# Optimization experiments

Hardware: AMD Instinct MI355X
Metric: run time of the kernel (lower is better)

The kernel has to match this reference:

```python
import jax, jax.numpy as jnp
import numpy as np

N_COMBIN, N_DEV, CONT, VOCAB, EMB = 50000, 100000, 62, 1000, 16
B, K, H, OUT, NCLS = 8192, 64, 4, 16, 1
FEAT = CONT + 2 * EMB  # 94
ALPHA = 0.2  # leaky relu slope


def setup_inputs() -> dict:
    key = jax.random.key(0)
    ks = jax.random.split(key, 32)
    rn = lambda k, shape, s=0.05: (jax.random.normal(k, shape, dtype=jnp.float32) * s)
    inp = {
        "combin_cont": jax.random.normal(ks[0], (N_COMBIN, CONT), jnp.float32),
        "combin_cat": jax.random.randint(ks[1], (N_COMBIN, 2), 0, VOCAB),
        "device_cont": jax.random.normal(ks[2], (N_DEV, CONT), jnp.float32),
        "device_cat": jax.random.randint(ks[3], (N_DEV, 2), 0, VOCAB),
        "combin_idx": jax.random.randint(ks[4], (B,), 0, N_COMBIN),
        "device_idx": jax.random.randint(ks[5], (B,), 0, N_DEV),
        "neighbor_idx": jax.random.randint(ks[6], (B, K), 0, N_DEV),
        "ce0": rn(ks[7], (VOCAB, EMB), 1.0),
        "ce1": rn(ks[8], (VOCAB, EMB), 1.0),
        "de0": rn(ks[9], (VOCAB, EMB), 1.0),
        "de1": rn(ks[10], (VOCAB, EMB), 1.0),
        "Wc": rn(ks[11], (H, FEAT, OUT)),
        "bc": rn(ks[12], (H, OUT)),
        "Wd": rn(ks[13], (H, FEAT, OUT)),
        "bd": rn(ks[14], (H, OUT)),
        "aW": rn(ks[15], (H, 2 * OUT)),
        "ab": rn(ks[16], (H,)),
        "W1": rn(ks[17], (H * OUT, OUT)),
        "b1": rn(ks[18], (OUT,)),
        "W2": rn(ks[19], (OUT + 2 * FEAT, 64)),
        "b2": rn(ks[20], (64,)),
        "W3": rn(ks[21], (64, 32)),
        "b3": rn(ks[22], (32,)),
        "W4": rn(ks[23], (32, NCLS)),
        "b4": rn(ks[24], (NCLS,)),
    }
    return inp


def reference(combin_cont, combin_cat, device_cont, device_cat,
              combin_idx, device_idx, neighbor_idx,
              ce0, ce1, de0, de1,
              Wc, bc, Wd, bd, aW, ab,
              W1, b1, W2, b2, W3, b3, W4, b4):
    # concat_embed_feats for device nodes: [N_dev, FEAT]
    dev_feats = jnp.concatenate(
        [device_cont, de0[device_cat[:, 0]], de1[device_cat[:, 1]]], axis=1)
    # combin batch features: [B, FEAT]
    cc = combin_cat[combin_idx]
    comb_batch = jnp.concatenate(
        [combin_cont[combin_idx], ce0[cc[:, 0]], ce1[cc[:, 1]]], axis=1)
    dev_batch = dev_feats[device_idx]            # [B, FEAT]
    neibr = dev_feats[neighbor_idx]              # [B, K, FEAT]

    # multi-head GAT attention (all heads vectorized)
    h_c = jnp.einsum('bf,hfo->bho', comb_batch, Wc) + bc[None]          # [B,H,OUT]
    h_n = jnp.einsum('bkf,hfo->bhko', neibr, Wd) + bd[None, :, None]    # [B,H,K,OUT]
    a1, a2 = aW[:, :OUT], aW[:, OUT:]
    e = (jnp.einsum('bho,ho->bh', h_c, a1)[:, :, None]
         + jnp.einsum('bhko,ho->bhk', h_n, a2)
         + ab[None, :, None])                                           # [B,H,K]
    e = jax.nn.leaky_relu(e, negative_slope=ALPHA)
    attn = jax.nn.softmax(e, axis=-1)
    head_out = jax.nn.elu(jnp.einsum('bhk,bhko->bho', attn, h_n))       # [B,H,OUT]
    attn_feats = head_out.reshape(head_out.shape[0], H * OUT) @ W1 + b1  # [B,OUT]

    fusion = jnp.concatenate([comb_batch, dev_batch, attn_feats], axis=1)
    x = jax.nn.relu(fusion @ W2 + b2)   # dropout is identity in eval
    x = jax.nn.relu(x @ W3 + b3)
    return jax.nn.sigmoid(x @ W4 + b4)  # [B, NCLS]
```

## Files before the change

kernel.cpp:

```cpp
#include <hip/hip_runtime.h>
#include <cmath>

#define NDEV   100000
#define NBATCH 8192
#define CONTF  62
#define EMB    16
#define FEAT   94
#define KNBR   64
#define NH     4
#define OUTD   16
#define HOUT   64
#define FUS    204
#define ALPHA  0.2f

#define NDEVG  1563
#define NCOMBG 128
#define KP     48

typedef unsigned short ushortT;
typedef unsigned int   uintT;
typedef ushortT ushort8v __attribute__((ext_vector_type(8)));
typedef short   short8  __attribute__((ext_vector_type(8)));
typedef float   float4v __attribute__((ext_vector_type(4)));


template <typename T>
__device__ __forceinline__ const T* uniform_ptr(const T* p) {
  uint64_t v = (uint64_t)(uintptr_t)p;
  uint32_t lo = __builtin_amdgcn_readfirstlane((uint32_t)v);
  uint32_t hi = __builtin_amdgcn_readfirstlane((uint32_t)(v >> 32));
  return (const T*)(uintptr_t)(((uint64_t)hi << 32) | lo);
}

__device__ __forceinline__ float bf2f(ushortT u) {
  return __uint_as_float(((unsigned int)u) << 16);
}
__device__ __forceinline__ ushortT f2bf(float f) {
  unsigned int i = __float_as_uint(f);
  unsigned int r = i + 0x7FFFu + ((i >> 16) & 1u);
  return (ushortT)(r >> 16);
}
__device__ __forceinline__ uintT pack2(float lo, float hi) {
  return ((uintT)f2bf(hi) << 16) | (uintT)f2bf(lo);
}

union FragU { uint4 u; short8 s; };

__global__ __launch_bounds__(256, 2) void k_feat(
    const float* __restrict__ device_cont, const int* __restrict__ device_cat,
    const float* __restrict__ de0, const float* __restrict__ de1,
    const float* __restrict__ Wd, const float* __restrict__ bd,
    const float* __restrict__ combin_cont, const int* __restrict__ combin_cat,
    const int* __restrict__ combin_idx,
    const float* __restrict__ ce0, const float* __restrict__ ce1,
    const float* __restrict__ Wc, const float* __restrict__ bc,
    const float* __restrict__ aW,
    ushortT* __restrict__ h_bf, float* __restrict__ e_d, float* __restrict__ e_c) {
  __shared__ uintT x_s[64 * KP];
  __shared__ uintT w_s[64 * KP];
  __shared__ int   ci_s[64];

  const int tid  = threadIdx.x;
  const int lane = tid & 63;
  const int wv = __builtin_amdgcn_readfirstlane((int)(tid >> 6));
  const int blk = blockIdx.x;
  const bool devp = blk < NDEVG;
  const int b0 = (devp ? blk : blk - NDEVG) * 64;

  if (!devp && tid < 64) ci_s[tid] = combin_idx[b0 + tid];

  {
    const float* __restrict__ Ws = devp ? Wd : Wc;
#pragma unroll 1
    for (int e = tid; e < 64 * 47; e += 256) {
      const int n = e & 63, p = e >> 6;
      const int h = n >> 4, o = n & 15;
      const float lo = Ws[(h * FEAT + 2 * p) * OUTD + o];
      const float hi = Ws[(h * FEAT + 2 * p + 1) * OUTD + o];
      w_s[n * KP + p] = pack2(lo, hi);
    }
    if (tid < 64) w_s[tid * KP + 47] = 0u;
  }
  __syncthreads();

  {
    const float* __restrict__ cont = devp ? device_cont : combin_cont;
#pragma unroll 1
    for (int e = tid; e < 64 * 31; e += 256) {
      const int r = e / 31, p = e - r * 31;
      const size_t srow = devp ? (size_t)min(b0 + r, NDEV - 1) : (size_t)ci_s[r];
      const float2 v = *reinterpret_cast<const float2*>(cont + srow * CONTF + 2 * p);
      x_s[r * KP + p] = pack2(v.x, v.y);
    }
  }
  if (tid < 128) {
    const int r = tid >> 1, tb = tid & 1;
    const int srow = devp ? min(b0 + r, NDEV - 1) : ci_s[r];
    const int cidx = (devp ? device_cat : combin_cat)[2 * srow + tb];
    const float* __restrict__ ep =
        (tb ? (devp ? de1 : ce1) : (devp ? de0 : ce0)) + (size_t)cidx * EMB;
    uintT* __restrict__ dst = &x_s[r * KP + 31 + tb * 8];
#pragma unroll
    for (int k4 = 0; k4 < 4; ++k4) {
      const float4 v = reinterpret_cast<const float4*>(ep)[k4];
      dst[2 * k4 + 0] = pack2(v.x, v.y);
      dst[2 * k4 + 1] = pack2(v.z, v.w);
    }
  }
  if (tid < 64) x_s[tid * KP + 47] = 0u;
  __syncthreads();

  const int m = lane & 15, q = lane >> 4;
  const float* bias = uniform_ptr(devp ? bd : bc);
  const float* aWl  = uniform_ptr(aW);

  float4v acc[NH];
#pragma unroll
  for (int ct = 0; ct < NH; ++ct) {
    const float bv = bias[ct * OUTD + m];
    acc[ct] = (float4v){bv, bv, bv, bv};
  }

  const uintT* xa = &x_s[(wv * 16 + m) * KP + q * 4];
#pragma unroll
  for (int c = 0; c < 3; ++c) {
    FragU af;
    af.u = *reinterpret_cast<const uint4*>(xa + c * 16);
#pragma unroll
    for (int ct = 0; ct < NH; ++ct) {
      FragU bf;
      bf.u = *reinterpret_cast<const uint4*>(&w_s[(ct * 16 + m) * KP + c * 16 + q * 4]);
      acc[ct] = __builtin_amdgcn_mfma_f32_16x16x32_bf16(af.s, bf.s, acc[ct], 0, 0, 0);
    }
  }

  const int aoff = devp ? OUTD : 0;
  float* __restrict__ eout = devp ? e_d : e_c;
#pragma unroll
  for (int ct = 0; ct < NH; ++ct) {
    const float av = aWl[ct * 2 * OUTD + aoff + m];
    float e0 = acc[ct][0] * av, e1 = acc[ct][1] * av,
          e2 = acc[ct][2] * av, e3 = acc[ct][3] * av;
#pragma unroll
    for (int msk = 1; msk < 16; msk <<= 1) {
      e0 += __shfl_xor(e0, msk);
      e1 += __shfl_xor(e1, msk);
      e2 += __shfl_xor(e2, msk);
      e3 += __shfl_xor(e3, msk);
    }
    if (m == ct) {
      const int row = b0 + wv * 16 + q * 4;
      const float ev[4] = {e0, e1, e2, e3};
#pragma unroll
      for (int r = 0; r < 4; ++r)
        if (!devp || row + r < NDEV) eout[(size_t)(row + r) * NH + ct] = ev[r];
    }
  }
  if (devp) {
#pragma unroll
    for (int ct = 0; ct < NH; ++ct) {
#pragma unroll
      for (int r = 0; r < 4; ++r) {
        const int row = b0 + wv * 16 + q * 4 + r;
        if (row < NDEV)
          h_bf[(size_t)row * HOUT + ct * OUTD + m] = f2bf(acc[ct][r]);
      }
    }
  }
}

__global__ __launch_bounds__(256, 4) void k_attn(
    const int* __restrict__ neighbor_idx, const int* __restrict__ device_idx,
    const int* __restrict__ device_cat, const float* __restrict__ device_cont,
    const float* __restrict__ de0, const float* __restrict__ de1,
    const int* __restrict__ combin_idx, const int* __restrict__ combin_cat,
    const float* __restrict__ combin_cont,
    const float* __restrict__ ce0, const float* __restrict__ ce1,
    const ushortT* __restrict__ h_bf, const float* __restrict__ e_d,
    const float* __restrict__ e_c, const float* __restrict__ ab,
    const float* __restrict__ W1, const float* __restrict__ b1,
    float* __restrict__ fus) {
  __shared__ __align__(16) float pb[4][NH][68];
  __shared__ __align__(16) int   nb[4][KNBR];
  __shared__ float hb[4][HOUT];
  __shared__ float afb[4][OUTD];

  const int lane = threadIdx.x & 63;
  const int wid  = __builtin_amdgcn_readfirstlane((int)(threadIdx.x >> 6));
  const int b    = blockIdx.x * 4 + wid;

  const int nk = neighbor_idx[(size_t)b * KNBR + lane];
  const float4 ed4 = *reinterpret_cast<const float4*>(e_d + (size_t)nk * NH);
  const float4 ec4 = *reinterpret_cast<const float4*>(e_c + (size_t)b * NH);
  const float4 ab4 = *reinterpret_cast<const float4*>(ab);

  float v0 = ec4.x + ed4.x + ab4.x;
  float v1 = ec4.y + ed4.y + ab4.y;
  float v2 = ec4.z + ed4.z + ab4.z;
  float v3 = ec4.w + ed4.w + ab4.w;
  v0 = v0 > 0.f ? v0 : ALPHA * v0;
  v1 = v1 > 0.f ? v1 : ALPHA * v1;
  v2 = v2 > 0.f ? v2 : ALPHA * v2;
  v3 = v3 > 0.f ? v3 : ALPHA * v3;

  float m0 = v0, m1 = v1, m2 = v2, m3 = v3;
#pragma unroll
  for (int msk = 1; msk < 64; msk <<= 1) {
    m0 = fmaxf(m0, __shfl_xor(m0, msk));
    m1 = fmaxf(m1, __shfl_xor(m1, msk));
    m2 = fmaxf(m2, __shfl_xor(m2, msk));
    m3 = fmaxf(m3, __shfl_xor(m3, msk));
  }
  float p0 = expf(v0 - m0), p1 = expf(v1 - m1), p2 = expf(v2 - m2), p3 = expf(v3 - m3);
  float s0 = p0, s1 = p1, s2 = p2, s3 = p3;
#pragma unroll
  for (int msk = 1; msk < 64; msk <<= 1) {
    s0 += __shfl_xor(s0, msk);
    s1 += __shfl_xor(s1, msk);
    s2 += __shfl_xor(s2, msk);
    s3 += __shfl_xor(s3, msk);
  }
  p0 /= s0; p1 /= s1; p2 /= s2; p3 /= s3;

  pb[wid][0][lane] = p0;
  pb[wid][1][lane] = p1;
  pb[wid][2][lane] = p2;
  pb[wid][3][lane] = p3;
  nb[wid][lane]    = nk;
  __syncthreads();

  {
    const int q = lane >> 3, c8 = lane & 7;
    const int hq = c8 >> 1;
    float a[8];
#pragma unroll
    for (int i = 0; i < 8; ++i) a[i] = 0.f;
#pragma unroll
    for (int t = 0; t < 8; ++t) {
      const int k   = q * 8 + t;
      const int n   = nb[wid][k];
      const float p = pb[wid][hq][k];
      const ushort8v hv =
          *reinterpret_cast<const ushort8v*>(h_bf + (size_t)n * HOUT + c8 * 8);
#pragma unroll
      for (int i = 0; i < 8; ++i) a[i] = fmaf(p, bf2f(hv[i]), a[i]);
    }
#pragma unroll
    for (int msk = 8; msk < 64; msk <<= 1) {
#pragma unroll
      for (int i = 0; i < 8; ++i) a[i] += __shfl_xor(a[i], msk);
    }
    if (q == 0) {
#pragma unroll
      for (int i = 0; i < 8; ++i) a[i] = a[i] > 0.f ? a[i] : expm1f(a[i]);
      float4* hp = reinterpret_cast<float4*>(&hb[wid][c8 * 8]);
      hp[0] = make_float4(a[0], a[1], a[2], a[3]);
      hp[1] = make_float4(a[4], a[5], a[6], a[7]);
    }
  }
  __syncthreads();

  {
    const int j = lane & 15, gg = lane >> 4;
    float part = 0.f;
#pragma unroll
    for (int t = 0; t < 16; ++t)
      part = fmaf(hb[wid][gg * 16 + t], W1[(gg * 16 + t) * OUTD + j], part);
    part += __shfl_xor(part, 16);
    part += __shfl_xor(part, 32);
    if (lane < 16) afb[wid][lane] = part + b1[lane];
  }
  __syncthreads();

  const int ci = combin_idx[b];
  const int cc0 = combin_cat[2 * ci], cc1 = combin_cat[2 * ci + 1];
  const int didx = device_idx[b];
  const int dc0 = device_cat[2 * didx], dc1 = device_cat[2 * didx + 1];
  float* __restrict__ frow = fus + (size_t)b * FUS;
#pragma unroll
  for (int t = 0; t < 4; ++t) {
    const int i = lane + t * 64;
    if (i < FUS) {
      float v;
      if (i < 62)       v = combin_cont[(size_t)ci * CONTF + i];
      else if (i < 78)  v = ce0[(size_t)cc0 * EMB + (i - 62)];
      else if (i < 94)  v = ce1[(size_t)cc1 * EMB + (i - 78)];
      else if (i < 156) v = device_cont[(size_t)didx * CONTF + (i - 94)];
      else if (i < 172) v = de0[(size_t)dc0 * EMB + (i - 156)];
      else if (i < 188) v = de1[(size_t)dc1 * EMB + (i - 172)];
      else              v = afb[wid][i - 188];
      frow[i] = v;
    }
  }
}

__global__ __launch_bounds__(256) void k_mlp(
    const float* __restrict__ fus,
    const float* __restrict__ W2, const float* __restrict__ b2,
    const float* __restrict__ W3, const float* __restrict__ b3,
    const float* __restrict__ W4, const float* __restrict__ b4,
    float* __restrict__ out) {
  __shared__ __align__(16) float part[4][4][64];
  __shared__ __align__(16) float x1s[2][4][64];
  const int tid  = threadIdx.x;
  const int lane = tid & 63;
  const int wid  = __builtin_amdgcn_readfirstlane((int)(tid >> 6));
  const int pair = wid >> 1, half = wid & 1;
  const int r0   = blockIdx.x * 8 + pair * 4;
  const int f0   = half * 102;

  const float* rp0 = uniform_ptr(fus + (size_t)(r0 + 0) * FUS + f0);
  const float* rp1 = uniform_ptr(fus + (size_t)(r0 + 1) * FUS + f0);
  const float* rp2 = uniform_ptr(fus + (size_t)(r0 + 2) * FUS + f0);
  const float* rp3 = uniform_ptr(fus + (size_t)(r0 + 3) * FUS + f0);

  float acc[4];
  const float bj = half ? 0.f : b2[lane];
#pragma unroll
  for (int r = 0; r < 4; ++r) acc[r] = bj;

#pragma unroll 1
  for (int c = 0; c < 17; ++c) {
#pragma unroll
    for (int k = 0; k < 6; ++k) {
      const int f = c * 6 + k;
      const float wv = W2[(f0 + f) * 64 + lane];
      acc[0] = fmaf(rp0[f], wv, acc[0]);
      acc[1] = fmaf(rp1[f], wv, acc[1]);
      acc[2] = fmaf(rp2[f], wv, acc[2]);
      acc[3] = fmaf(rp3[f], wv, acc[3]);
    }
  }
#pragma unroll
  for (int r = 0; r < 4; ++r) part[wid][r][lane] = acc[r];
  __syncthreads();

  if (half == 0) {
#pragma unroll
    for (int r = 0; r < 4; ++r)
      x1s[pair][r][lane] = fmaxf(part[wid][r][lane] + part[wid + 1][r][lane], 0.f);
  }
  __syncthreads();

  const int row = tid >> 5, m = tid & 31;
  const int pr = row >> 2, rr = row & 3;
  float x2 = b3[m];
#pragma unroll 2
  for (int j4 = 0; j4 < 16; ++j4) {
    const float4 xv = *reinterpret_cast<const float4*>(&x1s[pr][rr][4 * j4]);
    x2 = fmaf(xv.x, W3[(4 * j4 + 0) * 32 + m], x2);
    x2 = fmaf(xv.y, W3[(4 * j4 + 1) * 32 + m], x2);
    x2 = fmaf(xv.z, W3[(4 * j4 + 2) * 32 + m], x2);
    x2 = fmaf(xv.w, W3[(4 * j4 + 3) * 32 + m], x2);
  }
  float p3r = fmaxf(x2, 0.f) * W4[m];
#pragma unroll
  for (int msk = 1; msk < 32; msk <<= 1) p3r += __shfl_xor(p3r, msk);
  if (m == 0) {
    const float z = p3r + b4[0];
    out[(size_t)(blockIdx.x * 8 + row)] = 1.f / (1.f + expf(-z));
  }
}

extern "C" void kernel_launch(void* const* d_in, const int* in_sizes, int n_in,
                              void* d_out, int out_size, void* d_ws, size_t ws_size,
                              hipStream_t stream) {
  const float* combin_cont  = (const float*)d_in[0];
  const int*   combin_cat   = (const int*)d_in[1];
  const float* device_cont  = (const float*)d_in[2];
  const int*   device_cat   = (const int*)d_in[3];
  const int*   combin_idx   = (const int*)d_in[4];
  const int*   device_idx   = (const int*)d_in[5];
  const int*   neighbor_idx = (const int*)d_in[6];
  const float* ce0 = (const float*)d_in[7];
  const float* ce1 = (const float*)d_in[8];
  const float* de0 = (const float*)d_in[9];
  const float* de1 = (const float*)d_in[10];
  const float* Wc  = (const float*)d_in[11];
  const float* bc  = (const float*)d_in[12];
  const float* Wd  = (const float*)d_in[13];
  const float* bd  = (const float*)d_in[14];
  const float* aW  = (const float*)d_in[15];
  const float* ab  = (const float*)d_in[16];
  const float* W1  = (const float*)d_in[17];
  const float* b1  = (const float*)d_in[18];
  const float* W2  = (const float*)d_in[19];
  const float* b2  = (const float*)d_in[20];
  const float* W3  = (const float*)d_in[21];
  const float* b3  = (const float*)d_in[22];
  const float* W4  = (const float*)d_in[23];
  const float* b4  = (const float*)d_in[24];

  float* ws  = (float*)d_ws;
  ushortT* h_bf = (ushortT*)ws;
  float* e_d = ws + 3200000;
  float* e_c = ws + 3600000;
  float* fus = ws + 3632768;

  k_feat<<<NDEVG + NCOMBG, 256, 0, stream>>>(
      device_cont, device_cat, de0, de1, Wd, bd,
      combin_cont, combin_cat, combin_idx, ce0, ce1, Wc, bc, aW,
      h_bf, e_d, e_c);
  k_attn<<<2048, 256, 0, stream>>>(
      neighbor_idx, device_idx, device_cat, device_cont, de0, de1,
      combin_idx, combin_cat, combin_cont, ce0, ce1,
      h_bf, e_d, e_c, ab, W1, b1, fus);
  k_mlp<<<1024, 256, 0, stream>>>(fus, W2, b2, W3, b3, W4, b4, (float*)d_out);
}
```

Measured before the change: 181.5 us.

## Fuse MLP into attention kernel and prepack bf16 weights in a prep kernel

Measured after the change: 167.0 us. 8.0% less time.

```diff
diff --git a/kernel.cpp b/kernel.cpp
--- a/kernel.cpp
+++ b/kernel.cpp
@@ -46,15 +46,34 @@
 
 union FragU { uint4 u; short8 s; };
 
+__global__ __launch_bounds__(256) void k_prep(
+    const float* __restrict__ Wd, const float* __restrict__ Wc,
+    uintT* __restrict__ wpack) {
+  const int e = blockIdx.x * 256 + threadIdx.x;
+  if (e >= 2 * 64 * KP) return;
+  const bool dev = e < 64 * KP;
+  const int i = dev ? e : e - 64 * KP;
+  const int n = i / KP, p = i - n * KP;
+  const int h = n >> 4, o = n & 15;
+  const float* __restrict__ Ws = dev ? Wd : Wc;
+  uintT v = 0u;
+  if (p < 47) {
+    const float lo = Ws[(h * FEAT + 2 * p) * OUTD + o];
+    const float hi = Ws[(h * FEAT + 2 * p + 1) * OUTD + o];
+    v = pack2(lo, hi);
+  }
+  wpack[e] = v;
+}
+
 __global__ __launch_bounds__(256, 2) void k_feat(
     const float* __restrict__ device_cont, const int* __restrict__ device_cat,
     const float* __restrict__ de0, const float* __restrict__ de1,
-    const float* __restrict__ Wd, const float* __restrict__ bd,
+    const float* __restrict__ bd,
     const float* __restrict__ combin_cont, const int* __restrict__ combin_cat,
     const int* __restrict__ combin_idx,
     const float* __restrict__ ce0, const float* __restrict__ ce1,
-    const float* __restrict__ Wc, const float* __restrict__ bc,
-    const float* __restrict__ aW,
+    const float* __restrict__ bc,
+    const float* __restrict__ aW, const uintT* __restrict__ wpack,
     ushortT* __restrict__ h_bf, float* __restrict__ e_d, float* __restrict__ e_c) {
   __shared__ uintT x_s[64 * KP];
   __shared__ uintT w_s[64 * KP];
@@ -70,16 +89,11 @@
   if (!devp && tid < 64) ci_s[tid] = combin_idx[b0 + tid];
 
   {
-    const float* __restrict__ Ws = devp ? Wd : Wc;
-#pragma unroll 1
-    for (int e = tid; e < 64 * 47; e += 256) {
-      const int n = e & 63, p = e >> 6;
-      const int h = n >> 4, o = n & 15;
-      const float lo = Ws[(h * FEAT + 2 * p) * OUTD + o];
-      const float hi = Ws[(h * FEAT + 2 * p + 1) * OUTD + o];
-      w_s[n * KP + p] = pack2(lo, hi);
-    }
-    if (tid < 64) w_s[tid * KP + 47] = 0u;
+    const uint4* __restrict__ wp =
+        reinterpret_cast<const uint4*>(wpack + (devp ? 0 : 64 * KP));
+#pragma unroll
+    for (int t = 0; t < 3; ++t)
+      reinterpret_cast<uint4*>(w_s)[t * 256 + tid] = wp[t * 256 + tid];
   }
   __syncthreads();
 
@@ -179,11 +193,15 @@
     const ushortT* __restrict__ h_bf, const float* __restrict__ e_d,
     const float* __restrict__ e_c, const float* __restrict__ ab,
     const float* __restrict__ W1, const float* __restrict__ b1,
-    float* __restrict__ fus) {
+    const float* __restrict__ W2, const float* __restrict__ b2,
+    const float* __restrict__ W3, const float* __restrict__ b3,
+    const float* __restrict__ W4, const float* __restrict__ b4,
+    float* __restrict__ out) {
   __shared__ __align__(16) float pb[4][NH][68];
   __shared__ __align__(16) int   nb[4][KNBR];
-  __shared__ float hb[4][HOUT];
-  __shared__ float afb[4][OUTD];
+  __shared__ __align__(16) float hb[4][HOUT];
+  __shared__ __align__(16) float fusb[4][208];
+  __shared__ __align__(16) float x1b[4][64];
 
   const int lane = threadIdx.x & 63;
   const int wid  = __builtin_amdgcn_readfirstlane((int)(threadIdx.x >> 6));
@@ -227,6 +245,25 @@
   pb[wid][2][lane] = p2;
   pb[wid][3][lane] = p3;
   nb[wid][lane]    = nk;
+
+  const int ci = combin_idx[b];
+  const int cc0 = combin_cat[2 * ci], cc1 = combin_cat[2 * ci + 1];
+  const int didx = device_idx[b];
+  const int dc0 = device_cat[2 * didx], dc1 = device_cat[2 * didx + 1];
+#pragma unroll
+  for (int t = 0; t < 3; ++t) {
+    const int i = lane + t * 64;
+    if (i < 188) {
+      float v;
+      if (i < 62)       v = combin_cont[(size_t)ci * CONTF + i];
+      else if (i < 78)  v = ce0[(size_t)cc0 * EMB + (i - 62)];
+      else if (i < 94)  v = ce1[(size_t)cc1 * EMB + (i - 78)];
+      else if (i < 156) v = device_cont[(size_t)didx * CONTF + (i - 94)];
+      else if (i < 172) v = de0[(size_t)dc0 * EMB + (i - 156)];
+      else              v = de1[(size_t)dc1 * EMB + (i - 172)];
+      fusb[wid][i] = v;
+    }
+  }
   __syncthreads();
 
   {
@@ -268,97 +305,30 @@
       part = fmaf(hb[wid][gg * 16 + t], W1[(gg * 16 + t) * OUTD + j], part);
     part += __shfl_xor(part, 16);
     part += __shfl_xor(part, 32);
-    if (lane < 16) afb[wid][lane] = part + b1[lane];
-  }
-  __syncthreads();
-
-  const int ci = combin_idx[b];
-  const int cc0 = combin_cat[2 * ci], cc1 = combin_cat[2 * ci + 1];
-  const int didx = device_idx[b];
-  const int dc0 = device_cat[2 * didx], dc1 = device_cat[2 * didx + 1];
-  float* __restrict__ frow = fus + (size_t)b * FUS;
-#pragma unroll
-  for (int t = 0; t < 4; ++t) {
-    const int i = lane + t * 64;
-    if (i < FUS) {
-      float v;
-      if (i < 62)       v = combin_cont[(size_t)ci * CONTF + i];
-      else if (i < 78)  v = ce0[(size_t)cc0 * EMB + (i - 62)];
-      else if (i < 94)  v = ce1[(size_t)cc1 * EMB + (i - 78)];
-      else if (i < 156) v = device_cont[(size_t)didx * CONTF + (i - 94)];
-      else if (i < 172) v = de0[(size_t)dc0 * EMB + (i - 156)];
-      else if (i < 188) v = de1[(size_t)dc1 * EMB + (i - 172)];
-      else              v = afb[wid][i - 188];
-      frow[i] = v;
-    }
-  }
-}
-
-__global__ __launch_bounds__(256) void k_mlp(
-    const float* __restrict__ fus,
-    const float* __restrict__ W2, const float* __restrict__ b2,
-    const float* __restrict__ W3, const float* __restrict__ b3,
-    const float* __restrict__ W4, const float* __restrict__ b4,
-    float* __restrict__ out) {
-  __shared__ __align__(16) float part[4][4][64];
-  __shared__ __align__(16) float x1s[2][4][64];
-  const int tid  = threadIdx.x;
-  const int lane = tid & 63;
-  const int wid  = __builtin_amdgcn_readfirstlane((int)(tid >> 6));
-  const int pair = wid >> 1, half = wid & 1;
-  const int r0   = blockIdx.x * 8 + pair * 4;
-  const int f0   = half * 102;
-
-  const float* rp0 = uniform_ptr(fus + (size_t)(r0 + 0) * FUS + f0);
-  const float* rp1 = uniform_ptr(fus + (size_t)(r0 + 1) * FUS + f0);
-  const float* rp2 = uniform_ptr(fus + (size_t)(r0 + 2) * FUS + f0);
-  const float* rp3 = uniform_ptr(fus + (size_t)(r0 + 3) * FUS + f0);
-
-  float acc[4];
-  const float bj = half ? 0.f : b2[lane];
-#pragma unroll
-  for (int r = 0; r < 4; ++r) acc[r] = bj;
-
-#pragma unroll 1
-  for (int c = 0; c < 17; ++c) {
-#pragma unroll
-    for (int k = 0; k < 6; ++k) {
-      const int f = c * 6 + k;
-      const float wv = W2[(f0 + f) * 64 + lane];
-      acc[0] = fmaf(rp0[f], wv, acc[0]);
-      acc[1] = fmaf(rp1[f], wv, acc[1]);
-      acc[2] = fmaf(rp2[f], wv, acc[2]);
-      acc[3] = fmaf(rp3[f], wv, acc[3]);
-    }
-  }
-#pragma unroll
-  for (int r = 0; r < 4; ++r) part[wid][r][lane] = acc[r];
-  __syncthreads();
-
-  if (half == 0) {
-#pragma unroll
-    for (int r = 0; r < 4; ++r)
-      x1s[pair][r][lane] = fmaxf(part[wid][r][lane] + part[wid + 1][r][lane], 0.f);
-  }
-  __syncthreads();
-
-  const int row = tid >> 5, m = tid & 31;
-  const int pr = row >> 2, rr = row & 3;
-  float x2 = b3[m];
-#pragma unroll 2
-  for (int j4 = 0; j4 < 16; ++j4) {
-    const float4 xv = *reinterpret_cast<const float4*>(&x1s[pr][rr][4 * j4]);
-    x2 = fmaf(xv.x, W3[(4 * j4 + 0) * 32 + m], x2);
-    x2 = fmaf(xv.y, W3[(4 * j4 + 1) * 32 + m], x2);
-    x2 = fmaf(xv.z, W3[(4 * j4 + 2) * 32 + m], x2);
-    x2 = fmaf(xv.w, W3[(4 * j4 + 3) * 32 + m], x2);
-  }
-  float p3r = fmaxf(x2, 0.f) * W4[m];
-#pragma unroll
-  for (int msk = 1; msk < 32; msk <<= 1) p3r += __shfl_xor(p3r, msk);
-  if (m == 0) {
-    const float z = p3r + b4[0];
-    out[(size_t)(blockIdx.x * 8 + row)] = 1.f / (1.f + expf(-z));
+    if (lane < 16) fusb[wid][188 + lane] = part + b1[lane];
+  }
+  __syncthreads();
+
+  float acc = b2[lane];
+#pragma unroll 4
+  for (int f = 0; f < FUS; ++f)
+    acc = fmaf(fusb[wid][f], W2[f * 64 + lane], acc);
+  x1b[wid][lane] = fmaxf(acc, 0.f);
+
+  const int m = lane & 31, rh = lane >> 5;
+  float x2 = rh ? 0.f : b3[m];
+#pragma unroll 4
+  for (int j = 0; j < 32; ++j) {
+    const int jj = rh * 32 + j;
+    x2 = fmaf(x1b[wid][jj], W3[jj * 32 + m], x2);
+  }
+  x2 += __shfl_xor(x2, 32);
+  float pL3 = fmaxf(x2, 0.f) * W4[m];
+#pragma unroll
+  for (int msk = 1; msk < 32; msk <<= 1) pL3 += __shfl_xor(pL3, msk);
+  if (lane == 0) {
+    const float z = pL3 + b4[0];
+    out[b] = 1.f / (1.f + expf(-z));
   }
 }
 
@@ -395,15 +365,15 @@
   ushortT* h_bf = (ushortT*)ws;
   float* e_d = ws + 3200000;
   float* e_c = ws + 3600000;
-  float* fus = ws + 3632768;
-
+  uintT* wpack = (uintT*)(ws + 3632768);
+
+  k_prep<<<24, 256, 0, stream>>>(Wd, Wc, wpack);
   k_feat<<<NDEVG + NCOMBG, 256, 0, stream>>>(
-      device_cont, device_cat, de0, de1, Wd, bd,
-      combin_cont, combin_cat, combin_idx, ce0, ce1, Wc, bc, aW,
+      device_cont, device_cat, de0, de1, bd,
+      combin_cont, combin_cat, combin_idx, ce0, ce1, bc, aW, wpack,
       h_bf, e_d, e_c);
   k_attn<<<2048, 256, 0, stream>>>(
       neighbor_idx, device_idx, device_cat, device_cont, de0, de1,
       combin_idx, combin_cat, combin_cont, ce0, ce1,
-      h_bf, e_d, e_c, ab, W1, b1, fus);
-  k_mlp<<<1024, 256, 0, stream>>>(fus, W2, b2, W3, b3, W4, b4, (float*)d_out);
-}
+      h_bf, e_d, e_c, ab, W1, b1, W2, b2, W3, b3, W4, b4, (float*)d_out);
+}
```
